# Kernel optimization log

Hardware: AMD Instinct MI355X
Metric: run time of the kernel (lower is better)

## Reference

```python
import jax, jax.numpy as jnp
import numpy as np

TOP_K = 4
ALPHA = 1.702
LIMIT = 7.0


def setup_inputs() -> dict:
    key = jax.random.key(0)
    ks = jax.random.split(key, 7)
    B, S, H, I, E = 1, 512, 2880, 2880, 16
    s = 0.02
    return {
        "hidden_states": jax.random.normal(ks[0], (B, S, H), dtype=jnp.float32),
        "router_w": jax.random.normal(ks[1], (H, E), dtype=jnp.float32) * s,
        "router_b": jax.random.normal(ks[2], (E,), dtype=jnp.float32) * s,
        "gate_up_w": jax.random.normal(ks[3], (E, H, 2 * I), dtype=jnp.float32) * s,
        "gate_up_b": jax.random.normal(ks[4], (E, 2 * I), dtype=jnp.float32) * s,
        "down_w": jax.random.normal(ks[5], (E, I, H), dtype=jnp.float32) * s,
        "down_b": jax.random.normal(ks[6], (E, H), dtype=jnp.float32) * s,
    }


def reference(hidden_states, router_w, router_b, gate_up_w, gate_up_b, down_w, down_b):
    B, S, H = hidden_states.shape
    x = hidden_states.reshape(-1, H)                      # [T, H]
    T = x.shape[0]

    # Router: top-k + softmax over selected logits, scattered back to [T, E]
    router_logits = x @ router_w + router_b               # [T, E]
    top_v, top_i = jax.lax.top_k(router_logits, TOP_K)    # [T, K]
    top_v = jax.nn.softmax(top_v, axis=-1)
    router_scores = jnp.zeros_like(router_logits).at[
        jnp.arange(T)[:, None], top_i
    ].set(top_v)                                          # [T, E]

    # Dense all-experts GLU (matches the repeat-across-experts formulation)
    gate_up = jnp.einsum('th,ehd->etd', x, gate_up_w) + gate_up_b[:, None, :]  # [E, T, 2I]
    gate = gate_up[..., ::2]                              # [E, T, I]
    up = gate_up[..., 1::2]                               # [E, T, I]
    gate = jnp.minimum(gate, LIMIT)
    up = jnp.clip(up, -LIMIT, LIMIT)
    glu = gate * jax.nn.sigmoid(gate * ALPHA)
    expert_out = jnp.einsum('eti,eih->eth', (up + 1.0) * glu, down_w) + down_b[:, None, :]  # [E, T, H]

    # Masked combine with routing weights
    out = jnp.sum(expert_out * router_scores.T[:, :, None], axis=0)  # [T, H]
    return (out.reshape(B, S, H),)
```

## Files before the change

kernel.cpp:

```cpp
#include <hip/hip_runtime.h>
#include <hip/hip_bf16.h>

#define NTOK 512
#define HDIM 2880
#define NGU  5760
#define NEXP 16
#define KSTEPS 90
#define MT 160
#define MFR 10

typedef float  f32x4  __attribute__((ext_vector_type(4)));
typedef float  f32x2  __attribute__((ext_vector_type(2)));
typedef short  bf16x8 __attribute__((ext_vector_type(8)));

__device__ __forceinline__ unsigned short f2bf(float f) {
  union { float f; unsigned u; } a; a.f = f;
  unsigned r = a.u + 0x7FFFu + ((a.u >> 16) & 1u);
  return (unsigned short)(r >> 16);
}

__device__ __forceinline__ void lds_barrier() {
  asm volatile("s_waitcnt lgkmcnt(0)" ::: "memory");
  __builtin_amdgcn_s_barrier();
  asm volatile("" ::: "memory");
}


__global__ void k_zero(int* counts) {
  if (threadIdx.x < NEXP) counts[threadIdx.x] = 0;
}

__global__ __launch_bounds__(256) void k_router(
    const float* __restrict__ x, const float* __restrict__ rw,
    const float* __restrict__ rb, int* __restrict__ counts,
    int* __restrict__ top_e, float* __restrict__ top_w)
{
  const int t = blockIdx.x;
  const int tid = threadIdx.x;
  __shared__ float red[256][17];
  float acc[NEXP];
#pragma unroll
  for (int e = 0; e < NEXP; ++e) acc[e] = 0.f;
  const float* xr = x + (size_t)t * HDIM;
  for (int h = tid; h < HDIM; h += 256) {
    float xv = xr[h];
    const f32x4* wr = (const f32x4*)(rw + (size_t)h * NEXP);
#pragma unroll
    for (int q = 0; q < 4; ++q) {
      f32x4 w = wr[q];
#pragma unroll
      for (int j = 0; j < 4; ++j) acc[q*4+j] += xv * w[j];
    }
  }
#pragma unroll
  for (int e = 0; e < NEXP; ++e) red[tid][e] = acc[e];
  __syncthreads();
  for (int s = 128; s > 0; s >>= 1) {
    if (tid < s) {
#pragma unroll
      for (int e = 0; e < NEXP; ++e) red[tid][e] += red[tid + s][e];
    }
    __syncthreads();
  }
  if (tid == 0) {
    float v[NEXP];
#pragma unroll
    for (int e = 0; e < NEXP; ++e) v[e] = red[0][e] + rb[e];
    int mask = 0; float tv[4]; int ti[4];
    for (int k = 0; k < 4; ++k) {
      float best = -3.4e38f; int bi = 0;
      for (int e = 0; e < NEXP; ++e)
        if (!((mask >> e) & 1) && v[e] > best) { best = v[e]; bi = e; }
      mask |= 1 << bi; tv[k] = best; ti[k] = bi;
    }
    float s = 0.f, ex[4];
    for (int k = 0; k < 4; ++k) { ex[k] = __expf(tv[k] - tv[0]); s += ex[k]; }
    float inv = 1.f / s;
    for (int k = 0; k < 4; ++k) {
      top_e[t*4+k] = ti[k];
      top_w[t*4+k] = ex[k] * inv;
      atomicAdd(&counts[ti[k]], 1);
    }
  }
}

__global__ __launch_bounds__(64) void k_fill(
    const int* __restrict__ top_e, const float* __restrict__ top_w,
    const int* __restrict__ counts, int* __restrict__ seg,
    int* __restrict__ pair_tok, float* __restrict__ pair_w)
{
  const int e = blockIdx.x;
  const int lane = threadIdx.x;
  int base = 0;
  for (int i = 0; i < e; ++i) base += counts[i];
  if (lane == 0) {
    seg[e] = base;
    if (e == NEXP - 1) seg[NEXP] = base + counts[e];
  }
  for (int t0 = 0; t0 < NTOK; t0 += 64) {
    int t = t0 + lane;
    int my = -1;
#pragma unroll
    for (int k = 0; k < 4; ++k) if (top_e[t*4+k] == e) my = k;
    unsigned long long m = __ballot(my >= 0);
    if (my >= 0) {
      int pre = __popcll(m & ((1ull << lane) - 1ull));
      pair_tok[base + pre] = t;
      pair_w[base + pre] = top_w[t*4+my];
    }
    base += (int)__popcll(m);
  }
}

__global__ __launch_bounds__(256) void k_xbf16(
    const float* __restrict__ x, unsigned short* __restrict__ xb)
{
  int i = (blockIdx.x * 256 + threadIdx.x) * 8;
  f32x4 a = *(const f32x4*)(x + i);
  f32x4 b = *(const f32x4*)(x + i + 4);
  bf16x8 o;
#pragma unroll
  for (int j = 0; j < 4; ++j) { o[j] = (short)f2bf(a[j]); o[4+j] = (short)f2bf(b[j]); }
  *(bf16x8*)(xb + i) = o;
}

__global__ __launch_bounds__(256) void k_outinit(
    const int* __restrict__ top_e, const float* __restrict__ top_w,
    const float* __restrict__ db, float* __restrict__ out)
{
  const int t = blockIdx.x;
  const int tid = threadIdx.x;
  const int e0 = top_e[t*4+0], e1 = top_e[t*4+1], e2 = top_e[t*4+2], e3 = top_e[t*4+3];
  const float w0 = top_w[t*4+0], w1 = top_w[t*4+1], w2 = top_w[t*4+2], w3 = top_w[t*4+3];
  const float* b0 = db + (size_t)e0 * HDIM;
  const float* b1 = db + (size_t)e1 * HDIM;
  const float* b2 = db + (size_t)e2 * HDIM;
  const float* b3 = db + (size_t)e3 * HDIM;
  for (int h = tid; h < HDIM; h += 256)
    out[(size_t)t*HDIM + h] = w0*b0[h] + w1*b1[h] + w2*b2[h] + w3*b3[h];
}

__global__ __launch_bounds__(256, 2) void k_gateup(
    const unsigned short* __restrict__ xb, const float* __restrict__ gw,
    const float* __restrict__ gb, const int* __restrict__ seg,
    const int* __restrict__ pair_tok, const float* __restrict__ pair_w,
    unsigned short* __restrict__ act)
{
  const int e = blockIdx.z;
  const int segs = seg[e];
  const int n_e = seg[e+1] - segs;
  const int m0 = blockIdx.y * MT;
  if (m0 >= n_e) return;
  const int tid = threadIdx.x;
  const int lane = tid & 63;
  const int wid = tid >> 6;
  const int l15 = lane & 15, lg = lane >> 4;
  const int fcb = blockIdx.x * 128 + wid * 32;
  const int fcE = fcb + 2*l15;
  const int colf = min(2*fcb + 4*l15, NGU - 4);

  __shared__ unsigned short Alds[2][MT][40];

  const float* Bq = gw + (size_t)e * HDIM * NGU + colf + (size_t)lg * 8 * NGU;

  const unsigned short* sp0 = nullptr;
  const unsigned short* sp1 = nullptr;
  const int r0 = tid >> 1, h0 = tid & 1;
  const int r1 = (tid + 256) >> 1, h1 = tid & 1;
  if (m0 + r0 < n_e) sp0 = xb + (size_t)pair_tok[segs + m0 + r0] * HDIM + h0*16;
  if (tid < 2*MT - 256 && m0 + r1 < n_e)
    sp1 = xb + (size_t)pair_tok[segs + m0 + r1] * HDIM + h1*16;

  f32x4 accgE[MFR], accuE[MFR], accgO[MFR], accuO[MFR];
  {
    f32x4 b = __builtin_nontemporal_load((const f32x4*)(gb + (size_t)e * NGU + colf));
#pragma unroll
    for (int m = 0; m < MFR; ++m)
#pragma unroll
      for (int r = 0; r < 4; ++r) {
        accgE[m][r] = b[0]; accuE[m][r] = b[1];
        accgO[m][r] = b[2]; accuO[m][r] = b[3];
      }
  }

  auto stage = [&](int ks, int b) {
    bf16x8 z = {0,0,0,0,0,0,0,0};
    bf16x8 v0 = z, v1 = z;
    if (sp0) { v0 = *(const bf16x8*)(sp0 + ks*32); v1 = *(const bf16x8*)(sp0 + ks*32 + 8); }
    *(bf16x8*)&Alds[b][r0][h0*16]     = v0;
    *(bf16x8*)&Alds[b][r0][h0*16 + 8] = v1;
    if (tid < 2*MT - 256) {
      bf16x8 w0 = z, w1 = z;
      if (sp1) { w0 = *(const bf16x8*)(sp1 + ks*32); w1 = *(const bf16x8*)(sp1 + ks*32 + 8); }
      *(bf16x8*)&Alds[b][r1][h1*16]     = w0;
      *(bf16x8*)&Alds[b][r1][h1*16 + 8] = w1;
    }
  };

  f32x4 bA[8];
  auto loadB = [&](int ks) {
    const float* bp = Bq + (size_t)ks * 32 * NGU;
#pragma unroll
    for (int j = 0; j < 8; ++j)
      bA[j] = __builtin_nontemporal_load((const f32x4*)(bp + (size_t)j * NGU));
  };

  loadB(0);
  stage(0, 0);
  lds_barrier();
  int buf = 0;

  for (int ks = 0; ks < KSTEPS; ++ks) {
    if (ks + 1 < KSTEPS) stage(ks + 1, buf ^ 1);
    bf16x8 bgE, buE, bgO, buO;
#pragma unroll
    for (int j = 0; j < 8; ++j) {
      bgE[j] = (short)f2bf(bA[j][0]); buE[j] = (short)f2bf(bA[j][1]);
      bgO[j] = (short)f2bf(bA[j][2]); buO[j] = (short)f2bf(bA[j][3]);
    }
    if (ks + 1 < KSTEPS) loadB(ks + 1);
#pragma unroll
    for (int m = 0; m < MFR; ++m) {
      bf16x8 a = *(const bf16x8*)&Alds[buf][m*16 + l15][lg*8];
      accgE[m] = __builtin_amdgcn_mfma_f32_16x16x32_bf16(a, bgE, accgE[m], 0, 0, 0);
      accuE[m] = __builtin_amdgcn_mfma_f32_16x16x32_bf16(a, buE, accuE[m], 0, 0, 0);
      accgO[m] = __builtin_amdgcn_mfma_f32_16x16x32_bf16(a, bgO, accgO[m], 0, 0, 0);
      accuO[m] = __builtin_amdgcn_mfma_f32_16x16x32_bf16(a, buO, accuO[m], 0, 0, 0);
    }
    lds_barrier();
    buf ^= 1;
  }

  if (fcE < HDIM) {
#pragma unroll
    for (int m = 0; m < MFR; ++m) {
#pragma unroll
      for (int r = 0; r < 4; ++r) {
        int grow = m0 + m*16 + lg*4 + r;
        if (grow < n_e) {
          float pw = pair_w[segs + grow];
          float gE = fminf(accgE[m][r], 7.f);
          float uE = fminf(fmaxf(accuE[m][r], -7.f), 7.f);
          float avE = (uE + 1.f) * (gE / (1.f + __expf(-1.702f * gE))) * pw;
          float gO = fminf(accgO[m][r], 7.f);
          float uO = fminf(fmaxf(accuO[m][r], -7.f), 7.f);
          float avO = (uO + 1.f) * (gO / (1.f + __expf(-1.702f * gO))) * pw;
          unsigned pk = (unsigned)f2bf(avE) | ((unsigned)f2bf(avO) << 16);
          *(unsigned*)&act[(size_t)(segs + grow) * HDIM + fcE] = pk;
        }
      }
    }
  }
}

__global__ __launch_bounds__(256, 3) void k_down(
    const unsigned short* __restrict__ act, const float* __restrict__ dw,
    const int* __restrict__ seg, const int* __restrict__ pair_tok,
    float* __restrict__ out)
{
  const int e = blockIdx.z;
  const int segs = seg[e];
  const int n_e = seg[e+1] - segs;
  const int m0 = blockIdx.y * MT;
  if (m0 >= n_e) return;
  const int tid = threadIdx.x;
  const int lane = tid & 63;
  const int wid = tid >> 6;
  const int l15 = lane & 15, lg = lane >> 4;
  const int cb = blockIdx.x * 128 + wid * 32;
  const int cE = cb + 2*l15;
  const int colc = min(cE, HDIM - 2);

  __shared__ unsigned short Alds[2][MT][40];

  const float* Bq = dw + (size_t)e * HDIM * HDIM + colc + (size_t)lg * 8 * HDIM;

  const unsigned short* sp0 = nullptr;
  const unsigned short* sp1 = nullptr;
  const int r0 = tid >> 1, h0 = tid & 1;
  const int r1 = (tid + 256) >> 1, h1 = tid & 1;
  if (m0 + r0 < n_e) sp0 = act + (size_t)(segs + m0 + r0) * HDIM + h0*16;
  if (tid < 2*MT - 256 && m0 + r1 < n_e)
    sp1 = act + (size_t)(segs + m0 + r1) * HDIM + h1*16;

  f32x4 accE[MFR], accO[MFR];
#pragma unroll
  for (int m = 0; m < MFR; ++m)
#pragma unroll
    for (int r = 0; r < 4; ++r) { accE[m][r] = 0.f; accO[m][r] = 0.f; }

  auto stage = [&](int ks, int b) {
    bf16x8 z = {0,0,0,0,0,0,0,0};
    bf16x8 v0 = z, v1 = z;
    if (sp0) { v0 = *(const bf16x8*)(sp0 + ks*32); v1 = *(const bf16x8*)(sp0 + ks*32 + 8); }
    *(bf16x8*)&Alds[b][r0][h0*16]     = v0;
    *(bf16x8*)&Alds[b][r0][h0*16 + 8] = v1;
    if (tid < 2*MT - 256) {
      bf16x8 w0 = z, w1 = z;
      if (sp1) { w0 = *(const bf16x8*)(sp1 + ks*32); w1 = *(const bf16x8*)(sp1 + ks*32 + 8); }
      *(bf16x8*)&Alds[b][r1][h1*16]     = w0;
      *(bf16x8*)&Alds[b][r1][h1*16 + 8] = w1;
    }
  };

  f32x2 bA[8];
  auto loadB = [&](int ks) {
    const float* bp = Bq + (size_t)ks * 32 * HDIM;
#pragma unroll
    for (int j = 0; j < 8; ++j)
      bA[j] = __builtin_nontemporal_load((const f32x2*)(bp + (size_t)j * HDIM));
  };

  loadB(0);
  stage(0, 0);
  lds_barrier();
  int buf = 0;

  for (int ks = 0; ks < KSTEPS; ++ks) {
    if (ks + 1 < KSTEPS) stage(ks + 1, buf ^ 1);
    bf16x8 bfE, bfO;
#pragma unroll
    for (int j = 0; j < 8; ++j) { bfE[j] = (short)f2bf(bA[j][0]); bfO[j] = (short)f2bf(bA[j][1]); }
    if (ks + 1 < KSTEPS) loadB(ks + 1);
#pragma unroll
    for (int m = 0; m < MFR; ++m) {
      bf16x8 a = *(const bf16x8*)&Alds[buf][m*16 + l15][lg*8];
      accE[m] = __builtin_amdgcn_mfma_f32_16x16x32_bf16(a, bfE, accE[m], 0, 0, 0);
      accO[m] = __builtin_amdgcn_mfma_f32_16x16x32_bf16(a, bfO, accO[m], 0, 0, 0);
    }
    lds_barrier();
    buf ^= 1;
  }

  if (cE < HDIM) {
#pragma unroll
    for (int m = 0; m < MFR; ++m) {
#pragma unroll
      for (int r = 0; r < 4; ++r) {
        int grow = m0 + m*16 + lg*4 + r;
        if (grow < n_e) {
          int t = pair_tok[segs + grow];
          atomicAdd(out + (size_t)t * HDIM + cE,     accE[m][r]);
          atomicAdd(out + (size_t)t * HDIM + cE + 1, accO[m][r]);
        }
      }
    }
  }
}


extern "C" void kernel_launch(void* const* d_in, const int* in_sizes, int n_in,
                              void* d_out, int out_size, void* d_ws, size_t ws_size,
                              hipStream_t stream) {
  const float* x  = (const float*)d_in[0];
  const float* rw = (const float*)d_in[1];
  const float* rb = (const float*)d_in[2];
  const float* gw = (const float*)d_in[3];
  const float* gb = (const float*)d_in[4];
  const float* dw = (const float*)d_in[5];
  const float* db = (const float*)d_in[6];
  float* out = (float*)d_out;

  char* w = (char*)d_ws;
  int*   counts   = (int*)(w);
  int*   seg      = (int*)(w + 64);
  int*   top_e    = (int*)(w + 1024);
  float* top_w    = (float*)(w + 1024 + 8192);
  int*   pair_tok = (int*)(w + 1024 + 16384);
  float* pair_w   = (float*)(w + 1024 + 24576);
  unsigned short* xb  = (unsigned short*)(w + (1 << 20));
  unsigned short* act = (unsigned short*)(w + (8 << 20));

  k_zero<<<1, 64, 0, stream>>>(counts);
  k_router<<<NTOK, 256, 0, stream>>>(x, rw, rb, counts, top_e, top_w);
  k_fill<<<NEXP, 64, 0, stream>>>(top_e, top_w, counts, seg, pair_tok, pair_w);
  k_xbf16<<<(NTOK*HDIM)/(256*8), 256, 0, stream>>>(x, xb);
  k_outinit<<<NTOK, 256, 0, stream>>>(top_e, top_w, db, out);

  dim3 gg(23, 2, NEXP);
  k_gateup<<<gg, 256, 0, stream>>>(xb, gw, gb, seg, pair_tok, pair_w, act);

  dim3 gd(23, 2, NEXP);
  k_down<<<gd, 256, 0, stream>>>(act, dw, seg, pair_tok, out);
}
```

Baseline: 463.7 us.

## Split-K both expert GEMMs in two halves with separate activation kernel

Both the gate_up and down expert GEMMs now split the K dimension into two halves, which doubles the grid along z so more workgroups run concurrently on the device. Gate_up writes fp32 partial sums to a new workspace buffer, and a new k_act kernel adds the two partials, then applies clamp, GLU and the routing weight before writing bf16 activations. The down kernel presumably accumulates its two halves atomically into the output, and a dummy LDS pad limits occupancy. This trades extra global traffic for the partials, plus one more kernel launch, for better CU utilisation; the zeroing kernel is also folded into k_xbf16 to save a launch.

Measured after the change: 510.2 us. +10.0%, slower.

```diff
diff --git a/kernel.cpp b/kernel.cpp
--- a/kernel.cpp
+++ b/kernel.cpp
@@ -5,9 +5,10 @@
 #define HDIM 2880
 #define NGU  5760
 #define NEXP 16
-#define KSTEPS 90
+#define KSH  45
 #define MT 160
 #define MFR 10
+#define GUELT ((size_t)(NTOK*4) * NGU)
 
 typedef float  f32x4  __attribute__((ext_vector_type(4)));
 typedef float  f32x2  __attribute__((ext_vector_type(2)));
@@ -25,10 +26,6 @@
   asm volatile("" ::: "memory");
 }
 
-
-__global__ void k_zero(int* counts) {
-  if (threadIdx.x < NEXP) counts[threadIdx.x] = 0;
-}
 
 __global__ __launch_bounds__(256) void k_router(
     const float* __restrict__ x, const float* __restrict__ rw,
@@ -113,8 +110,10 @@
 }
 
 __global__ __launch_bounds__(256) void k_xbf16(
-    const float* __restrict__ x, unsigned short* __restrict__ xb)
-{
+    const float* __restrict__ x, unsigned short* __restrict__ xb,
+    int* __restrict__ counts)
+{
+  if (blockIdx.x == 0 && threadIdx.x < NEXP) counts[threadIdx.x] = 0;
   int i = (blockIdx.x * 256 + threadIdx.x) * 8;
   f32x4 a = *(const f32x4*)(x + i);
   f32x4 b = *(const f32x4*)(x + i + 4);
@@ -143,10 +142,10 @@
 __global__ __launch_bounds__(256, 2) void k_gateup(
     const unsigned short* __restrict__ xb, const float* __restrict__ gw,
     const float* __restrict__ gb, const int* __restrict__ seg,
-    const int* __restrict__ pair_tok, const float* __restrict__ pair_w,
-    unsigned short* __restrict__ act)
-{
-  const int e = blockIdx.z;
+    const int* __restrict__ pair_tok, float* __restrict__ gu)
+{
+  const int e  = blockIdx.z >> 1;
+  const int kh = blockIdx.z & 1;
   const int segs = seg[e];
   const int n_e = seg[e+1] - segs;
   const int m0 = blockIdx.y * MT;
@@ -160,20 +159,27 @@
   const int colf = min(2*fcb + 4*l15, NGU - 4);
 
   __shared__ unsigned short Alds[2][MT][40];
-
-  const float* Bq = gw + (size_t)e * HDIM * NGU + colf + (size_t)lg * 8 * NGU;
+  __shared__ char lds_pad[29 << 10];
+  if (__builtin_expect(seg == nullptr, 0)) lds_pad[tid] = 1;
+
+  float* gup = gu + (size_t)kh * GUELT;
+  const float* Bq = gw + (size_t)e * HDIM * NGU + colf
+                  + (size_t)(kh * (KSH*32) + lg * 8) * NGU;
 
   const unsigned short* sp0 = nullptr;
   const unsigned short* sp1 = nullptr;
   const int r0 = tid >> 1, h0 = tid & 1;
   const int r1 = (tid + 256) >> 1, h1 = tid & 1;
-  if (m0 + r0 < n_e) sp0 = xb + (size_t)pair_tok[segs + m0 + r0] * HDIM + h0*16;
+  if (m0 + r0 < n_e)
+    sp0 = xb + (size_t)pair_tok[segs + m0 + r0] * HDIM + kh*(KSH*32) + h0*16;
   if (tid < 2*MT - 256 && m0 + r1 < n_e)
-    sp1 = xb + (size_t)pair_tok[segs + m0 + r1] * HDIM + h1*16;
+    sp1 = xb + (size_t)pair_tok[segs + m0 + r1] * HDIM + kh*(KSH*32) + h1*16;
 
   f32x4 accgE[MFR], accuE[MFR], accgO[MFR], accuO[MFR];
   {
-    f32x4 b = __builtin_nontemporal_load((const f32x4*)(gb + (size_t)e * NGU + colf));
+    f32x4 b = {0.f, 0.f, 0.f, 0.f};
+    if (kh == 0)
+      b = __builtin_nontemporal_load((const f32x4*)(gb + (size_t)e * NGU + colf));
 #pragma unroll
     for (int m = 0; m < MFR; ++m)
 #pragma unroll
@@ -210,15 +216,15 @@
   lds_barrier();
   int buf = 0;
 
-  for (int ks = 0; ks < KSTEPS; ++ks) {
-    if (ks + 1 < KSTEPS) stage(ks + 1, buf ^ 1);
+  for (int ks = 0; ks < KSH; ++ks) {
+    if (ks + 1 < KSH) stage(ks + 1, buf ^ 1);
     bf16x8 bgE, buE, bgO, buO;
 #pragma unroll
     for (int j = 0; j < 8; ++j) {
       bgE[j] = (short)f2bf(bA[j][0]); buE[j] = (short)f2bf(bA[j][1]);
       bgO[j] = (short)f2bf(bA[j][2]); buO[j] = (short)f2bf(bA[j][3]);
     }
-    if (ks + 1 < KSTEPS) loadB(ks + 1);
+    if (ks + 1 < KSH) loadB(ks + 1);
 #pragma unroll
     for (int m = 0; m < MFR; ++m) {
       bf16x8 a = *(const bf16x8*)&Alds[buf][m*16 + l15][lg*8];
@@ -238,27 +244,44 @@
       for (int r = 0; r < 4; ++r) {
         int grow = m0 + m*16 + lg*4 + r;
         if (grow < n_e) {
-          float pw = pair_w[segs + grow];
-          float gE = fminf(accgE[m][r], 7.f);
-          float uE = fminf(fmaxf(accuE[m][r], -7.f), 7.f);
-          float avE = (uE + 1.f) * (gE / (1.f + __expf(-1.702f * gE))) * pw;
-          float gO = fminf(accgO[m][r], 7.f);
-          float uO = fminf(fmaxf(accuO[m][r], -7.f), 7.f);
-          float avO = (uO + 1.f) * (gO / (1.f + __expf(-1.702f * gO))) * pw;
-          unsigned pk = (unsigned)f2bf(avE) | ((unsigned)f2bf(avO) << 16);
-          *(unsigned*)&act[(size_t)(segs + grow) * HDIM + fcE] = pk;
+          f32x4 v = { accgE[m][r], accuE[m][r], accgO[m][r], accuO[m][r] };
+          *(f32x4*)&gup[(size_t)(segs + grow) * NGU + colf] = v;
         }
       }
     }
   }
 }
 
-__global__ __launch_bounds__(256, 3) void k_down(
+__global__ __launch_bounds__(256) void k_act(
+    const float* __restrict__ gu, const float* __restrict__ pair_w,
+    unsigned short* __restrict__ act)
+{
+  const int row = blockIdx.x;
+  const float w = pair_w[row];
+  const float* a = gu + (size_t)row * NGU;
+  const float* b = gu + GUELT + (size_t)row * NGU;
+  unsigned short* o = act + (size_t)row * HDIM;
+  for (int p = threadIdx.x; p < HDIM/2; p += 256) {
+    f32x4 va = *(const f32x4*)(a + 4*p);
+    f32x4 vb = *(const f32x4*)(b + 4*p);
+    float g0 = va[0] + vb[0], u0 = va[1] + vb[1];
+    float g1 = va[2] + vb[2], u1 = va[3] + vb[3];
+    g0 = fminf(g0, 7.f); u0 = fminf(fmaxf(u0, -7.f), 7.f);
+    g1 = fminf(g1, 7.f); u1 = fminf(fmaxf(u1, -7.f), 7.f);
+    float av0 = (u0 + 1.f) * (g0 / (1.f + __expf(-1.702f * g0))) * w;
+    float av1 = (u1 + 1.f) * (g1 / (1.f + __expf(-1.702f * g1))) * w;
+    unsigned pk = (unsigned)f2bf(av0) | ((unsigned)f2bf(av1) << 16);
+    *(unsigned*)&o[2*p] = pk;
+  }
+}
+
+__global__ __launch_bounds__(256, 2) void k_down(
     const unsigned short* __restrict__ act, const float* __restrict__ dw,
     const int* __restrict__ seg, const int* __restrict__ pair_tok,
     float* __restrict__ out)
 {
-  const int e = blockIdx.z;
+  const int e  = blockIdx.z >> 1;
+  const int kh = blockIdx.z & 1;
   const int segs = seg[e];
   const int n_e = seg[e+1] - segs;
   const int m0 = blockIdx.y * MT;
@@ -272,16 +295,20 @@
   const int colc = min(cE, HDIM - 2);
 
   __shared__ unsigned short Alds[2][MT][40];
-
-  const float* Bq = dw + (size_t)e * HDIM * HDIM + colc + (size_t)lg * 8 * HDIM;
+  __shared__ char lds_pad[29 << 10];
+  if (__builtin_expect(seg == nullptr, 0)) lds_pad[tid] = 1;
+
+  const float* Bq = dw + (size_t)e * HDIM * HDIM + colc
+                  + (size_t)(kh * (KSH*32) + lg * 8) * HDIM;
 
   const unsigned short* sp0 = nullptr;
   const unsigned short* sp1 = nullptr;
   const int r0 = tid >> 1, h0 = tid & 1;
   const int r1 = (tid + 256) >> 1, h1 = tid & 1;
-  if (m0 + r0 < n_e) sp0 = act + (size_t)(segs + m0 + r0) * HDIM + h0*16;
+  if (m0 + r0 < n_e)
+    sp0 = act + (size_t)(segs + m0 + r0) * HDIM + kh*(KSH*32) + h0*16;
   if (tid < 2*MT - 256 && m0 + r1 < n_e)
-    sp1 = act + (size_t)(segs + m0 + r1) * HDIM + h1*16;
+    sp1 = act + (size_t)(segs + m0 + r1) * HDIM + kh*(KSH*32) + h1*16;
 
   f32x4 accE[MFR], accO[MFR];
 #pragma unroll
@@ -316,12 +343,12 @@
   lds_barrier();
   int buf = 0;
 
-  for (int ks = 0; ks < KSTEPS; ++ks) {
-    if (ks + 1 < KSTEPS) stage(ks + 1, buf ^ 1);
+  for (int ks = 0; ks < KSH; ++ks) {
+    if (ks + 1 < KSH) stage(ks + 1, buf ^ 1);
     bf16x8 bfE, bfO;
 #pragma unroll
     for (int j = 0; j < 8; ++j) { bfE[j] = (short)f2bf(bA[j][0]); bfO[j] = (short)f2bf(bA[j][1]); }
-    if (ks + 1 < KSTEPS) loadB(ks + 1);
+    if (ks + 1 < KSH) loadB(ks + 1);
 #pragma unroll
     for (int m = 0; m < MFR; ++m) {
       bf16x8 a = *(const bf16x8*)&Alds[buf][m*16 + l15][lg*8];
@@ -370,16 +397,18 @@
   float* pair_w   = (float*)(w + 1024 + 24576);
   unsigned short* xb  = (unsigned short*)(w + (1 << 20));
   unsigned short* act = (unsigned short*)(w + (8 << 20));
-
-  k_zero<<<1, 64, 0, stream>>>(counts);
+  float* gu = (float*)(w + (64ull << 20));
+
+  k_xbf16<<<(NTOK*HDIM)/(256*8), 256, 0, stream>>>(x, xb, counts);
   k_router<<<NTOK, 256, 0, stream>>>(x, rw, rb, counts, top_e, top_w);
   k_fill<<<NEXP, 64, 0, stream>>>(top_e, top_w, counts, seg, pair_tok, pair_w);
-  k_xbf16<<<(NTOK*HDIM)/(256*8), 256, 0, stream>>>(x, xb);
   k_outinit<<<NTOK, 256, 0, stream>>>(top_e, top_w, db, out);
 
-  dim3 gg(23, 2, NEXP);
-  k_gateup<<<gg, 256, 0, stream>>>(xb, gw, gb, seg, pair_tok, pair_w, act);
-
-  dim3 gd(23, 2, NEXP);
+  dim3 gg(23, 2, NEXP * 2);
+  k_gateup<<<gg, 256, 0, stream>>>(xb, gw, gb, seg, pair_tok, gu);
+
+  k_act<<<NTOK*4, 256, 0, stream>>>(gu, pair_w, act);
+
+  dim3 gd(23, 2, NEXP * 2);
   k_down<<<gd, 256, 0, stream>>>(act, dw, seg, pair_tok, out);
 }
```

## Fuse gate-up and down GEMMs into persistent kernel with per-expert dependency counters

Applied to the files above, without the earlier changes.

Replaces the separate gate-up and down launches with one persistent kernel of 512 blocks that pulls work items from an atomic queue. Gate-up items come first, and each down item spins until all gate-up tiles of its expert have signalled completion. This lets one expert's down projection overlap other experts' gate-up work and removes the tail gap between the two kernels. It also folds the counter zeroing into the conversion kernel to drop one launch. The costs are spin-wait latency, an atomic fetch per item, and a bounded-guard spin that could silently proceed on a timeout.

New measurement: 804.7 us. +73.5%, slower.

```diff
diff --git a/kernel.cpp b/kernel.cpp
--- a/kernel.cpp
+++ b/kernel.cpp
@@ -8,6 +8,8 @@
 #define KSTEPS 90
 #define MT 160
 #define MFR 10
+#define NITEM_G 736
+#define NITEM_ALL (2*NITEM_G)
 
 typedef float  f32x4  __attribute__((ext_vector_type(4)));
 typedef float  f32x2  __attribute__((ext_vector_type(2)));
@@ -25,10 +27,6 @@
   asm volatile("" ::: "memory");
 }
 
-
-__global__ void k_zero(int* counts) {
-  if (threadIdx.x < NEXP) counts[threadIdx.x] = 0;
-}
 
 __global__ __launch_bounds__(256) void k_router(
     const float* __restrict__ x, const float* __restrict__ rw,
@@ -87,10 +85,13 @@
 __global__ __launch_bounds__(64) void k_fill(
     const int* __restrict__ top_e, const float* __restrict__ top_w,
     const int* __restrict__ counts, int* __restrict__ seg,
-    int* __restrict__ pair_tok, float* __restrict__ pair_w)
+    int* __restrict__ pair_tok, float* __restrict__ pair_w,
+    int* __restrict__ qhead, int* __restrict__ done)
 {
   const int e = blockIdx.x;
   const int lane = threadIdx.x;
+  if (lane == 1) done[e] = 0;
+  if (e == 0 && lane == 2) *qhead = 0;
   int base = 0;
   for (int i = 0; i < e; ++i) base += counts[i];
   if (lane == 0) {
@@ -113,8 +114,10 @@
 }
 
 __global__ __launch_bounds__(256) void k_xbf16(
-    const float* __restrict__ x, unsigned short* __restrict__ xb)
-{
+    const float* __restrict__ x, unsigned short* __restrict__ xb,
+    int* __restrict__ counts)
+{
+  if (blockIdx.x == 0 && threadIdx.x < NEXP) counts[threadIdx.x] = 0;
   int i = (blockIdx.x * 256 + threadIdx.x) * 8;
   f32x4 a = *(const f32x4*)(x + i);
   f32x4 b = *(const f32x4*)(x + i + 4);
@@ -140,208 +143,219 @@
     out[(size_t)t*HDIM + h] = w0*b0[h] + w1*b1[h] + w2*b2[h] + w3*b3[h];
 }
 
-__global__ __launch_bounds__(256, 2) void k_gateup(
+__global__ __launch_bounds__(256, 2) void k_fused(
     const unsigned short* __restrict__ xb, const float* __restrict__ gw,
-    const float* __restrict__ gb, const int* __restrict__ seg,
-    const int* __restrict__ pair_tok, const float* __restrict__ pair_w,
-    unsigned short* __restrict__ act)
-{
-  const int e = blockIdx.z;
-  const int segs = seg[e];
-  const int n_e = seg[e+1] - segs;
-  const int m0 = blockIdx.y * MT;
-  if (m0 >= n_e) return;
+    const float* __restrict__ gb, const float* __restrict__ dw,
+    const int* __restrict__ seg, const int* __restrict__ pair_tok,
+    const float* __restrict__ pair_w, unsigned short* __restrict__ act,
+    float* __restrict__ out, int* __restrict__ qhead, int* __restrict__ done)
+{
+  __shared__ unsigned short Alds[2][MT][40];
+  __shared__ int s_id;
   const int tid = threadIdx.x;
   const int lane = tid & 63;
   const int wid = tid >> 6;
   const int l15 = lane & 15, lg = lane >> 4;
-  const int fcb = blockIdx.x * 128 + wid * 32;
-  const int fcE = fcb + 2*l15;
-  const int colf = min(2*fcb + 4*l15, NGU - 4);
-
-  __shared__ unsigned short Alds[2][MT][40];
-
-  const float* Bq = gw + (size_t)e * HDIM * NGU + colf + (size_t)lg * 8 * NGU;
-
-  const unsigned short* sp0 = nullptr;
-  const unsigned short* sp1 = nullptr;
   const int r0 = tid >> 1, h0 = tid & 1;
   const int r1 = (tid + 256) >> 1, h1 = tid & 1;
-  if (m0 + r0 < n_e) sp0 = xb + (size_t)pair_tok[segs + m0 + r0] * HDIM + h0*16;
-  if (tid < 2*MT - 256 && m0 + r1 < n_e)
-    sp1 = xb + (size_t)pair_tok[segs + m0 + r1] * HDIM + h1*16;
-
-  f32x4 accgE[MFR], accuE[MFR], accgO[MFR], accuO[MFR];
-  {
-    f32x4 b = __builtin_nontemporal_load((const f32x4*)(gb + (size_t)e * NGU + colf));
-#pragma unroll
-    for (int m = 0; m < MFR; ++m)
-#pragma unroll
-      for (int r = 0; r < 4; ++r) {
-        accgE[m][r] = b[0]; accuE[m][r] = b[1];
-        accgO[m][r] = b[2]; accuO[m][r] = b[3];
-      }
-  }
-
-  auto stage = [&](int ks, int b) {
-    bf16x8 z = {0,0,0,0,0,0,0,0};
-    bf16x8 v0 = z, v1 = z;
-    if (sp0) { v0 = *(const bf16x8*)(sp0 + ks*32); v1 = *(const bf16x8*)(sp0 + ks*32 + 8); }
-    *(bf16x8*)&Alds[b][r0][h0*16]     = v0;
-    *(bf16x8*)&Alds[b][r0][h0*16 + 8] = v1;
-    if (tid < 2*MT - 256) {
-      bf16x8 w0 = z, w1 = z;
-      if (sp1) { w0 = *(const bf16x8*)(sp1 + ks*32); w1 = *(const bf16x8*)(sp1 + ks*32 + 8); }
-      *(bf16x8*)&Alds[b][r1][h1*16]     = w0;
-      *(bf16x8*)&Alds[b][r1][h1*16 + 8] = w1;
-    }
-  };
-
-  f32x4 bA[8];
-  auto loadB = [&](int ks) {
-    const float* bp = Bq + (size_t)ks * 32 * NGU;
-#pragma unroll
-    for (int j = 0; j < 8; ++j)
-      bA[j] = __builtin_nontemporal_load((const f32x4*)(bp + (size_t)j * NGU));
-  };
-
-  loadB(0);
-  stage(0, 0);
-  lds_barrier();
-  int buf = 0;
-
-  for (int ks = 0; ks < KSTEPS; ++ks) {
-    if (ks + 1 < KSTEPS) stage(ks + 1, buf ^ 1);
-    bf16x8 bgE, buE, bgO, buO;
-#pragma unroll
-    for (int j = 0; j < 8; ++j) {
-      bgE[j] = (short)f2bf(bA[j][0]); buE[j] = (short)f2bf(bA[j][1]);
-      bgO[j] = (short)f2bf(bA[j][2]); buO[j] = (short)f2bf(bA[j][3]);
-    }
-    if (ks + 1 < KSTEPS) loadB(ks + 1);
-#pragma unroll
-    for (int m = 0; m < MFR; ++m) {
-      bf16x8 a = *(const bf16x8*)&Alds[buf][m*16 + l15][lg*8];
-      accgE[m] = __builtin_amdgcn_mfma_f32_16x16x32_bf16(a, bgE, accgE[m], 0, 0, 0);
-      accuE[m] = __builtin_amdgcn_mfma_f32_16x16x32_bf16(a, buE, accuE[m], 0, 0, 0);
-      accgO[m] = __builtin_amdgcn_mfma_f32_16x16x32_bf16(a, bgO, accgO[m], 0, 0, 0);
-      accuO[m] = __builtin_amdgcn_mfma_f32_16x16x32_bf16(a, buO, accuO[m], 0, 0, 0);
-    }
-    lds_barrier();
-    buf ^= 1;
-  }
-
-  if (fcE < HDIM) {
-#pragma unroll
-    for (int m = 0; m < MFR; ++m) {
-#pragma unroll
-      for (int r = 0; r < 4; ++r) {
-        int grow = m0 + m*16 + lg*4 + r;
-        if (grow < n_e) {
-          float pw = pair_w[segs + grow];
-          float gE = fminf(accgE[m][r], 7.f);
-          float uE = fminf(fmaxf(accuE[m][r], -7.f), 7.f);
-          float avE = (uE + 1.f) * (gE / (1.f + __expf(-1.702f * gE))) * pw;
-          float gO = fminf(accgO[m][r], 7.f);
-          float uO = fminf(fmaxf(accuO[m][r], -7.f), 7.f);
-          float avO = (uO + 1.f) * (gO / (1.f + __expf(-1.702f * gO))) * pw;
-          unsigned pk = (unsigned)f2bf(avE) | ((unsigned)f2bf(avO) << 16);
-          *(unsigned*)&act[(size_t)(segs + grow) * HDIM + fcE] = pk;
-        }
-      }
-    }
-  }
-}
-
-__global__ __launch_bounds__(256, 3) void k_down(
-    const unsigned short* __restrict__ act, const float* __restrict__ dw,
-    const int* __restrict__ seg, const int* __restrict__ pair_tok,
-    float* __restrict__ out)
-{
-  const int e = blockIdx.z;
-  const int segs = seg[e];
-  const int n_e = seg[e+1] - segs;
-  const int m0 = blockIdx.y * MT;
-  if (m0 >= n_e) return;
-  const int tid = threadIdx.x;
-  const int lane = tid & 63;
-  const int wid = tid >> 6;
-  const int l15 = lane & 15, lg = lane >> 4;
-  const int cb = blockIdx.x * 128 + wid * 32;
-  const int cE = cb + 2*l15;
-  const int colc = min(cE, HDIM - 2);
-
-  __shared__ unsigned short Alds[2][MT][40];
-
-  const float* Bq = dw + (size_t)e * HDIM * HDIM + colc + (size_t)lg * 8 * HDIM;
-
-  const unsigned short* sp0 = nullptr;
-  const unsigned short* sp1 = nullptr;
-  const int r0 = tid >> 1, h0 = tid & 1;
-  const int r1 = (tid + 256) >> 1, h1 = tid & 1;
-  if (m0 + r0 < n_e) sp0 = act + (size_t)(segs + m0 + r0) * HDIM + h0*16;
-  if (tid < 2*MT - 256 && m0 + r1 < n_e)
-    sp1 = act + (size_t)(segs + m0 + r1) * HDIM + h1*16;
-
-  f32x4 accE[MFR], accO[MFR];
-#pragma unroll
-  for (int m = 0; m < MFR; ++m)
-#pragma unroll
-    for (int r = 0; r < 4; ++r) { accE[m][r] = 0.f; accO[m][r] = 0.f; }
-
-  auto stage = [&](int ks, int b) {
-    bf16x8 z = {0,0,0,0,0,0,0,0};
-    bf16x8 v0 = z, v1 = z;
-    if (sp0) { v0 = *(const bf16x8*)(sp0 + ks*32); v1 = *(const bf16x8*)(sp0 + ks*32 + 8); }
-    *(bf16x8*)&Alds[b][r0][h0*16]     = v0;
-    *(bf16x8*)&Alds[b][r0][h0*16 + 8] = v1;
-    if (tid < 2*MT - 256) {
-      bf16x8 w0 = z, w1 = z;
-      if (sp1) { w0 = *(const bf16x8*)(sp1 + ks*32); w1 = *(const bf16x8*)(sp1 + ks*32 + 8); }
-      *(bf16x8*)&Alds[b][r1][h1*16]     = w0;
-      *(bf16x8*)&Alds[b][r1][h1*16 + 8] = w1;
-    }
-  };
-
-  f32x2 bA[8];
-  auto loadB = [&](int ks) {
-    const float* bp = Bq + (size_t)ks * 32 * HDIM;
-#pragma unroll
-    for (int j = 0; j < 8; ++j)
-      bA[j] = __builtin_nontemporal_load((const f32x2*)(bp + (size_t)j * HDIM));
-  };
-
-  loadB(0);
-  stage(0, 0);
-  lds_barrier();
-  int buf = 0;
-
-  for (int ks = 0; ks < KSTEPS; ++ks) {
-    if (ks + 1 < KSTEPS) stage(ks + 1, buf ^ 1);
-    bf16x8 bfE, bfO;
-#pragma unroll
-    for (int j = 0; j < 8; ++j) { bfE[j] = (short)f2bf(bA[j][0]); bfO[j] = (short)f2bf(bA[j][1]); }
-    if (ks + 1 < KSTEPS) loadB(ks + 1);
-#pragma unroll
-    for (int m = 0; m < MFR; ++m) {
-      bf16x8 a = *(const bf16x8*)&Alds[buf][m*16 + l15][lg*8];
-      accE[m] = __builtin_amdgcn_mfma_f32_16x16x32_bf16(a, bfE, accE[m], 0, 0, 0);
-      accO[m] = __builtin_amdgcn_mfma_f32_16x16x32_bf16(a, bfO, accO[m], 0, 0, 0);
-    }
-    lds_barrier();
-    buf ^= 1;
-  }
-
-  if (cE < HDIM) {
-#pragma unroll
-    for (int m = 0; m < MFR; ++m) {
-#pragma unroll
-      for (int r = 0; r < 4; ++r) {
-        int grow = m0 + m*16 + lg*4 + r;
-        if (grow < n_e) {
-          int t = pair_tok[segs + grow];
-          atomicAdd(out + (size_t)t * HDIM + cE,     accE[m][r]);
-          atomicAdd(out + (size_t)t * HDIM + cE + 1, accO[m][r]);
+
+  for (;;) {
+    __syncthreads();
+    if (tid == 0) s_id = atomicAdd(qhead, 1);
+    __syncthreads();
+    const int id = s_id;
+    if (id >= NITEM_ALL) break;
+
+    const bool is_dn = id >= NITEM_G;
+    const int rid = is_dn ? id - NITEM_G : id;
+    const int e  = rid / 46;
+    const int y  = (rid % 46) / 23;
+    const int ct = rid % 23;
+    const int segs = seg[e];
+    const int n_e = seg[e+1] - segs;
+    const int m0 = y * MT;
+    if (m0 >= n_e) continue;
+
+    if (!is_dn) {
+      const int fcb = ct * 128 + wid * 32;
+      const int fcE = fcb + 2*l15;
+      const int colf = min(2*fcb + 4*l15, NGU - 4);
+      const float* Bq = gw + (size_t)e * HDIM * NGU + colf + (size_t)lg * 8 * NGU;
+
+      const unsigned short* sp0 = nullptr;
+      const unsigned short* sp1 = nullptr;
+      if (m0 + r0 < n_e) sp0 = xb + (size_t)pair_tok[segs + m0 + r0] * HDIM + h0*16;
+      else sp0 = nullptr;
+      if (tid < 2*MT - 256 && m0 + r1 < n_e)
+        sp1 = xb + (size_t)pair_tok[segs + m0 + r1] * HDIM + h1*16;
+
+      f32x4 accgE[MFR], accuE[MFR], accgO[MFR], accuO[MFR];
+      {
+        f32x4 b = __builtin_nontemporal_load((const f32x4*)(gb + (size_t)e * NGU + colf));
+#pragma unroll
+        for (int m = 0; m < MFR; ++m)
+#pragma unroll
+          for (int r = 0; r < 4; ++r) {
+            accgE[m][r] = b[0]; accuE[m][r] = b[1];
+            accgO[m][r] = b[2]; accuO[m][r] = b[3];
+          }
+      }
+
+      auto stage = [&](int ks, int b) {
+        bf16x8 z = {0,0,0,0,0,0,0,0};
+        bf16x8 v0 = z, v1 = z;
+        if (sp0) { v0 = *(const bf16x8*)(sp0 + ks*32); v1 = *(const bf16x8*)(sp0 + ks*32 + 8); }
+        *(bf16x8*)&Alds[b][r0][h0*16]     = v0;
+        *(bf16x8*)&Alds[b][r0][h0*16 + 8] = v1;
+        if (tid < 2*MT - 256) {
+          bf16x8 w0 = z, w1 = z;
+          if (sp1) { w0 = *(const bf16x8*)(sp1 + ks*32); w1 = *(const bf16x8*)(sp1 + ks*32 + 8); }
+          *(bf16x8*)&Alds[b][r1][h1*16]     = w0;
+          *(bf16x8*)&Alds[b][r1][h1*16 + 8] = w1;
+        }
+      };
+
+      f32x4 bA[8];
+      auto loadB = [&](int ks) {
+        const float* bp = Bq + (size_t)ks * 32 * NGU;
+#pragma unroll
+        for (int j = 0; j < 8; ++j)
+          bA[j] = __builtin_nontemporal_load((const f32x4*)(bp + (size_t)j * NGU));
+      };
+
+      loadB(0);
+      stage(0, 0);
+      lds_barrier();
+      int buf = 0;
+
+      for (int ks = 0; ks < KSTEPS; ++ks) {
+        if (ks + 1 < KSTEPS) stage(ks + 1, buf ^ 1);
+        bf16x8 bgE, buE, bgO, buO;
+#pragma unroll
+        for (int j = 0; j < 8; ++j) {
+          bgE[j] = (short)f2bf(bA[j][0]); buE[j] = (short)f2bf(bA[j][1]);
+          bgO[j] = (short)f2bf(bA[j][2]); buO[j] = (short)f2bf(bA[j][3]);
+        }
+        if (ks + 1 < KSTEPS) loadB(ks + 1);
+#pragma unroll
+        for (int m = 0; m < MFR; ++m) {
+          bf16x8 a = *(const bf16x8*)&Alds[buf][m*16 + l15][lg*8];
+          accgE[m] = __builtin_amdgcn_mfma_f32_16x16x32_bf16(a, bgE, accgE[m], 0, 0, 0);
+          accuE[m] = __builtin_amdgcn_mfma_f32_16x16x32_bf16(a, buE, accuE[m], 0, 0, 0);
+          accgO[m] = __builtin_amdgcn_mfma_f32_16x16x32_bf16(a, bgO, accgO[m], 0, 0, 0);
+          accuO[m] = __builtin_amdgcn_mfma_f32_16x16x32_bf16(a, buO, accuO[m], 0, 0, 0);
+        }
+        lds_barrier();
+        buf ^= 1;
+      }
+
+      if (fcE < HDIM) {
+#pragma unroll
+        for (int m = 0; m < MFR; ++m) {
+#pragma unroll
+          for (int r = 0; r < 4; ++r) {
+            int grow = m0 + m*16 + lg*4 + r;
+            if (grow < n_e) {
+              float pw = pair_w[segs + grow];
+              float gE = fminf(accgE[m][r], 7.f);
+              float uE = fminf(fmaxf(accuE[m][r], -7.f), 7.f);
+              float avE = (uE + 1.f) * (gE / (1.f + __expf(-1.702f * gE))) * pw;
+              float gO = fminf(accgO[m][r], 7.f);
+              float uO = fminf(fmaxf(accuO[m][r], -7.f), 7.f);
+              float avO = (uO + 1.f) * (gO / (1.f + __expf(-1.702f * gO))) * pw;
+              unsigned pk = (unsigned)f2bf(avE) | ((unsigned)f2bf(avO) << 16);
+              *(unsigned*)&act[(size_t)(segs + grow) * HDIM + fcE] = pk;
+            }
+          }
+        }
+      }
+      __syncthreads();
+      if (tid == 0)
+        __hip_atomic_fetch_add(done + e, 1, __ATOMIC_RELEASE, __HIP_MEMORY_SCOPE_AGENT);
+    } else {
+      const int target = 23 * ((n_e + MT - 1) / MT);
+      if (tid == 0) {
+        int guard = 0;
+        while (__hip_atomic_load(done + e, __ATOMIC_ACQUIRE, __HIP_MEMORY_SCOPE_AGENT) < target) {
+          __builtin_amdgcn_s_sleep(32);
+          if (++guard > (1 << 22)) break;
+        }
+      }
+      __syncthreads();
+      __threadfence();
+
+      const int cb = ct * 128 + wid * 32;
+      const int cE = cb + 2*l15;
+      const int colc = min(cE, HDIM - 2);
+      const float* Bq = dw + (size_t)e * HDIM * HDIM + colc + (size_t)lg * 8 * HDIM;
+
+      const unsigned short* sp0 = nullptr;
+      const unsigned short* sp1 = nullptr;
+      if (m0 + r0 < n_e) sp0 = act + (size_t)(segs + m0 + r0) * HDIM + h0*16;
+      if (tid < 2*MT - 256 && m0 + r1 < n_e)
+        sp1 = act + (size_t)(segs + m0 + r1) * HDIM + h1*16;
+
+      f32x4 accE[MFR], accO[MFR];
+#pragma unroll
+      for (int m = 0; m < MFR; ++m)
+#pragma unroll
+        for (int r = 0; r < 4; ++r) { accE[m][r] = 0.f; accO[m][r] = 0.f; }
+
+      auto stage = [&](int ks, int b) {
+        bf16x8 z = {0,0,0,0,0,0,0,0};
+        bf16x8 v0 = z, v1 = z;
+        if (sp0) { v0 = *(const bf16x8*)(sp0 + ks*32); v1 = *(const bf16x8*)(sp0 + ks*32 + 8); }
+        *(bf16x8*)&Alds[b][r0][h0*16]     = v0;
+        *(bf16x8*)&Alds[b][r0][h0*16 + 8] = v1;
+        if (tid < 2*MT - 256) {
+          bf16x8 w0 = z, w1 = z;
+          if (sp1) { w0 = *(const bf16x8*)(sp1 + ks*32); w1 = *(const bf16x8*)(sp1 + ks*32 + 8); }
+          *(bf16x8*)&Alds[b][r1][h1*16]     = w0;
+          *(bf16x8*)&Alds[b][r1][h1*16 + 8] = w1;
+        }
+      };
+
+      f32x2 bA[8];
+      auto loadB = [&](int ks) {
+        const float* bp = Bq + (size_t)ks * 32 * HDIM;
+#pragma unroll
+        for (int j = 0; j < 8; ++j)
+          bA[j] = __builtin_nontemporal_load((const f32x2*)(bp + (size_t)j * HDIM));
+      };
+
+      loadB(0);
+      stage(0, 0);
+      lds_barrier();
+      int buf = 0;
+
+      for (int ks = 0; ks < KSTEPS; ++ks) {
+        if (ks + 1 < KSTEPS) stage(ks + 1, buf ^ 1);
+        bf16x8 bfE, bfO;
+#pragma unroll
+        for (int j = 0; j < 8; ++j) { bfE[j] = (short)f2bf(bA[j][0]); bfO[j] = (short)f2bf(bA[j][1]); }
+        if (ks + 1 < KSTEPS) loadB(ks + 1);
+#pragma unroll
+        for (int m = 0; m < MFR; ++m) {
+          bf16x8 a = *(const bf16x8*)&Alds[buf][m*16 + l15][lg*8];
+          accE[m] = __builtin_amdgcn_mfma_f32_16x16x32_bf16(a, bfE, accE[m], 0, 0, 0);
+          accO[m] = __builtin_amdgcn_mfma_f32_16x16x32_bf16(a, bfO, accO[m], 0, 0, 0);
+        }
+        lds_barrier();
+        buf ^= 1;
+      }
+
+      if (cE < HDIM) {
+#pragma unroll
+        for (int m = 0; m < MFR; ++m) {
+#pragma unroll
+          for (int r = 0; r < 4; ++r) {
+            int grow = m0 + m*16 + lg*4 + r;
+            if (grow < n_e) {
+              int t = pair_tok[segs + grow];
+              atomicAdd(out + (size_t)t * HDIM + cE,     accE[m][r]);
+              atomicAdd(out + (size_t)t * HDIM + cE + 1, accO[m][r]);
+            }
+          }
         }
       }
     }
@@ -363,7 +377,9 @@
 
   char* w = (char*)d_ws;
   int*   counts   = (int*)(w);
-  int*   seg      = (int*)(w + 64);
+  int*   qhead    = (int*)(w + 256);
+  int*   done     = (int*)(w + 512);
+  int*   seg      = (int*)(w + 640);
   int*   top_e    = (int*)(w + 1024);
   float* top_w    = (float*)(w + 1024 + 8192);
   int*   pair_tok = (int*)(w + 1024 + 16384);
@@ -371,15 +387,11 @@
   unsigned short* xb  = (unsigned short*)(w + (1 << 20));
   unsigned short* act = (unsigned short*)(w + (8 << 20));
 
-  k_zero<<<1, 64, 0, stream>>>(counts);
+  k_xbf16<<<(NTOK*HDIM)/(256*8), 256, 0, stream>>>(x, xb, counts);
   k_router<<<NTOK, 256, 0, stream>>>(x, rw, rb, counts, top_e, top_w);
-  k_fill<<<NEXP, 64, 0, stream>>>(top_e, top_w, counts, seg, pair_tok, pair_w);
-  k_xbf16<<<(NTOK*HDIM)/(256*8), 256, 0, stream>>>(x, xb);
+  k_fill<<<NEXP, 64, 0, stream>>>(top_e, top_w, counts, seg, pair_tok, pair_w, qhead, done);
   k_outinit<<<NTOK, 256, 0, stream>>>(top_e, top_w, db, out);
 
-  dim3 gg(23, 2, NEXP);
-  k_gateup<<<gg, 256, 0, stream>>>(xb, gw, gb, seg, pair_tok, pair_w, act);
-
-  dim3 gd(23, 2, NEXP);
-  k_down<<<gd, 256, 0, stream>>>(act, dw, seg, pair_tok, out);
-}
+  k_fused<<<512, 256, 0, stream>>>(xb, gw, gb, dw, seg, pair_tok, pair_w,
+                                   act, out, qhead, done);
+}
```

## Replace atomic scatter in down projection with partial buffer and gather kernel

Applied to the files above, without the earlier changes.

The down-projection kernel now writes per-pair results into a partial buffer instead of doing float atomicAdds into the output. A new gather kernel sums the four expert partials per token and adds the weighted biases, which replaces the old output-init kernel. The counts zeroing is folded into the bf16 conversion kernel to drop one launch. This removes atomic contention and gives deterministic sums, at the cost of an extra partial buffer write and read plus one more kernel.

Result: faster. 447.4 us (-3.5%).

```diff
diff --git a/kernel.cpp b/kernel.cpp
--- a/kernel.cpp
+++ b/kernel.cpp
@@ -26,10 +26,6 @@
 }
 
 
-__global__ void k_zero(int* counts) {
-  if (threadIdx.x < NEXP) counts[threadIdx.x] = 0;
-}
-
 __global__ __launch_bounds__(256) void k_router(
     const float* __restrict__ x, const float* __restrict__ rw,
     const float* __restrict__ rb, int* __restrict__ counts,
@@ -87,7 +83,8 @@
 __global__ __launch_bounds__(64) void k_fill(
     const int* __restrict__ top_e, const float* __restrict__ top_w,
     const int* __restrict__ counts, int* __restrict__ seg,
-    int* __restrict__ pair_tok, float* __restrict__ pair_w)
+    int* __restrict__ pair_tok, float* __restrict__ pair_w,
+    int* __restrict__ pair_of)
 {
   const int e = blockIdx.x;
   const int lane = threadIdx.x;
@@ -107,14 +104,17 @@
       int pre = __popcll(m & ((1ull << lane) - 1ull));
       pair_tok[base + pre] = t;
       pair_w[base + pre] = top_w[t*4+my];
+      pair_of[t*4 + my] = base + pre;
     }
     base += (int)__popcll(m);
   }
 }
 
 __global__ __launch_bounds__(256) void k_xbf16(
-    const float* __restrict__ x, unsigned short* __restrict__ xb)
-{
+    const float* __restrict__ x, unsigned short* __restrict__ xb,
+    int* __restrict__ counts)
+{
+  if (blockIdx.x == 0 && threadIdx.x < NEXP) counts[threadIdx.x] = 0;
   int i = (blockIdx.x * 256 + threadIdx.x) * 8;
   f32x4 a = *(const f32x4*)(x + i);
   f32x4 b = *(const f32x4*)(x + i + 4);
@@ -122,22 +122,6 @@
 #pragma unroll
   for (int j = 0; j < 4; ++j) { o[j] = (short)f2bf(a[j]); o[4+j] = (short)f2bf(b[j]); }
   *(bf16x8*)(xb + i) = o;
-}
-
-__global__ __launch_bounds__(256) void k_outinit(
-    const int* __restrict__ top_e, const float* __restrict__ top_w,
-    const float* __restrict__ db, float* __restrict__ out)
-{
-  const int t = blockIdx.x;
-  const int tid = threadIdx.x;
-  const int e0 = top_e[t*4+0], e1 = top_e[t*4+1], e2 = top_e[t*4+2], e3 = top_e[t*4+3];
-  const float w0 = top_w[t*4+0], w1 = top_w[t*4+1], w2 = top_w[t*4+2], w3 = top_w[t*4+3];
-  const float* b0 = db + (size_t)e0 * HDIM;
-  const float* b1 = db + (size_t)e1 * HDIM;
-  const float* b2 = db + (size_t)e2 * HDIM;
-  const float* b3 = db + (size_t)e3 * HDIM;
-  for (int h = tid; h < HDIM; h += 256)
-    out[(size_t)t*HDIM + h] = w0*b0[h] + w1*b1[h] + w2*b2[h] + w3*b3[h];
 }
 
 __global__ __launch_bounds__(256, 2) void k_gateup(
@@ -256,7 +240,7 @@
 __global__ __launch_bounds__(256, 3) void k_down(
     const unsigned short* __restrict__ act, const float* __restrict__ dw,
     const int* __restrict__ seg, const int* __restrict__ pair_tok,
-    float* __restrict__ out)
+    float* __restrict__ partial)
 {
   const int e = blockIdx.z;
   const int segs = seg[e];
@@ -339,12 +323,49 @@
       for (int r = 0; r < 4; ++r) {
         int grow = m0 + m*16 + lg*4 + r;
         if (grow < n_e) {
-          int t = pair_tok[segs + grow];
-          atomicAdd(out + (size_t)t * HDIM + cE,     accE[m][r]);
-          atomicAdd(out + (size_t)t * HDIM + cE + 1, accO[m][r]);
+          f32x2 v = { accE[m][r], accO[m][r] };
+          *(f32x2*)&partial[(size_t)(segs + grow) * HDIM + cE] = v;
         }
       }
     }
+  }
+}
+
+__global__ __launch_bounds__(256) void k_gather(
+    const float* __restrict__ partial, const int* __restrict__ pair_of,
+    const int* __restrict__ top_e, const float* __restrict__ top_w,
+    const float* __restrict__ db, float* __restrict__ out)
+{
+  const int t = blockIdx.x;
+  const int tid = threadIdx.x;
+  const int p0 = pair_of[t*4+0], p1 = pair_of[t*4+1];
+  const int p2 = pair_of[t*4+2], p3 = pair_of[t*4+3];
+  const float w0 = top_w[t*4+0], w1 = top_w[t*4+1];
+  const float w2 = top_w[t*4+2], w3 = top_w[t*4+3];
+  const float* r0 = partial + (size_t)p0 * HDIM;
+  const float* r1 = partial + (size_t)p1 * HDIM;
+  const float* r2 = partial + (size_t)p2 * HDIM;
+  const float* r3 = partial + (size_t)p3 * HDIM;
+  const float* b0 = db + (size_t)top_e[t*4+0] * HDIM;
+  const float* b1 = db + (size_t)top_e[t*4+1] * HDIM;
+  const float* b2 = db + (size_t)top_e[t*4+2] * HDIM;
+  const float* b3 = db + (size_t)top_e[t*4+3] * HDIM;
+  float* o = out + (size_t)t * HDIM;
+  for (int p = tid; p < HDIM/4; p += 256) {
+    f32x4 v0 = *(const f32x4*)(r0 + 4*p);
+    f32x4 v1 = *(const f32x4*)(r1 + 4*p);
+    f32x4 v2 = *(const f32x4*)(r2 + 4*p);
+    f32x4 v3 = *(const f32x4*)(r3 + 4*p);
+    f32x4 c0 = *(const f32x4*)(b0 + 4*p);
+    f32x4 c1 = *(const f32x4*)(b1 + 4*p);
+    f32x4 c2 = *(const f32x4*)(b2 + 4*p);
+    f32x4 c3 = *(const f32x4*)(b3 + 4*p);
+    f32x4 s;
+#pragma unroll
+    for (int j = 0; j < 4; ++j)
+      s[j] = (v0[j] + v1[j]) + (v2[j] + v3[j])
+           + (w0*c0[j] + w1*c1[j]) + (w2*c2[j] + w3*c3[j]);
+    *(f32x4*)(o + 4*p) = s;
   }
 }
 
@@ -368,18 +389,20 @@
   float* top_w    = (float*)(w + 1024 + 8192);
   int*   pair_tok = (int*)(w + 1024 + 16384);
   float* pair_w   = (float*)(w + 1024 + 24576);
+  int*   pair_of  = (int*)(w + 1024 + 32768);
   unsigned short* xb  = (unsigned short*)(w + (1 << 20));
   unsigned short* act = (unsigned short*)(w + (8 << 20));
-
-  k_zero<<<1, 64, 0, stream>>>(counts);
+  float* partial = (float*)(w + (64ull << 20));
+
+  k_xbf16<<<(NTOK*HDIM)/(256*8), 256, 0, stream>>>(x, xb, counts);
   k_router<<<NTOK, 256, 0, stream>>>(x, rw, rb, counts, top_e, top_w);
-  k_fill<<<NEXP, 64, 0, stream>>>(top_e, top_w, counts, seg, pair_tok, pair_w);
-  k_xbf16<<<(NTOK*HDIM)/(256*8), 256, 0, stream>>>(x, xb);
-  k_outinit<<<NTOK, 256, 0, stream>>>(top_e, top_w, db, out);
+  k_fill<<<NEXP, 64, 0, stream>>>(top_e, top_w, counts, seg, pair_tok, pair_w, pair_of);
 
   dim3 gg(23, 2, NEXP);
   k_gateup<<<gg, 256, 0, stream>>>(xb, gw, gb, seg, pair_tok, pair_w, act);
 
   dim3 gd(23, 2, NEXP);
-  k_down<<<gd, 256, 0, stream>>>(act, dw, seg, pair_tok, out);
-}
+  k_down<<<gd, 256, 0, stream>>>(act, dw, seg, pair_tok, partial);
+
+  k_gather<<<NTOK, 256, 0, stream>>>(partial, pair_of, top_e, top_w, db, out);
+}
```
